# Kernel tuning notes

Hardware: AMD Instinct MI355X
Metric: run time of the kernel (lower is better)

Reference implementation:

```python
import math
import jax, jax.numpy as jnp
import numpy as np

B, C, H, W = 2, 512, 64, 64
HEADS = 8            # channels // num_head_channels = 512 // 64
GROUPS = 32
EPS = 1e-6


def setup_inputs() -> dict:
    key = jax.random.key(0)
    ks = jax.random.split(key, 7)
    x = jax.random.normal(ks[0], (B, C, H, W), dtype=jnp.float32)
    gamma = 1.0 + 0.02 * jax.random.normal(ks[1], (C,), dtype=jnp.float32)
    beta = 0.02 * jax.random.normal(ks[2], (C,), dtype=jnp.float32)
    w_qkv = jax.random.normal(ks[3], (3 * C, C), dtype=jnp.float32) / math.sqrt(C)
    b_qkv = 0.02 * jax.random.normal(ks[4], (3 * C,), dtype=jnp.float32)
    # proj_out is zero-initialized in the module; use small random weights so the
    # op is numerically non-trivial (trained-checkpoint regime)
    w_proj = jax.random.normal(ks[5], (C, C), dtype=jnp.float32) / math.sqrt(C)
    b_proj = 0.02 * jax.random.normal(ks[6], (C,), dtype=jnp.float32)
    return {"x": x, "gamma": gamma, "beta": beta, "w_qkv": w_qkv,
            "b_qkv": b_qkv, "w_proj": w_proj, "b_proj": b_proj}


def reference(x, gamma, beta, w_qkv, b_qkv, w_proj, b_proj):
    b, c, h, w = x.shape
    L = h * w
    xr = x.reshape(b, c, L)

    # GroupNorm(32) over (channels_per_group, spatial)
    xg = xr.reshape(b, GROUPS, c // GROUPS, L)
    mu = jnp.mean(xg, axis=(2, 3), keepdims=True)
    var = jnp.var(xg, axis=(2, 3), keepdims=True)
    xn = ((xg - mu) * jax.lax.rsqrt(var + EPS)).reshape(b, c, L)
    xn = xn * gamma[:, None] + beta[:, None]

    # 1x1 conv QKV: [b, 3c, L]
    qkv = jnp.einsum('oc,bcl->bol', w_qkv, xn) + b_qkv[:, None]

    # QKVAttentionLegacy: reshape [b,3c,L] -> [b*heads, 3*ch, L], split q,k,v
    ch = c // HEADS
    qkv = qkv.reshape(b * HEADS, 3 * ch, L)
    q, k, v = jnp.split(qkv, 3, axis=1)
    scale = 1.0 / math.sqrt(math.sqrt(ch))
    weight = jnp.einsum('bct,bcs->bts', q * scale, k * scale)  # [b*H, L, L]
    weight = jax.nn.softmax(weight.astype(jnp.float32), axis=-1).astype(qkv.dtype)
    a = jnp.einsum('bts,bcs->bct', weight, v).reshape(b, c, L)

    # zero-initialized (here random) 1x1 proj + residual
    hproj = jnp.einsum('oc,bcl->bol', w_proj, a) + b_proj[:, None]
    return (xr + hproj).reshape(b, c, h, w)
```

## Files before the change

### kernel.cpp

```cpp
#include <hip/hip_runtime.h>
#include <stdint.h>


#define LTOK 4096
#define CDIM 512
#define NHEADS 8
#define EPS_GN 1e-6f
#define QKSCALE 0.3535533905932738f
#define QSCL (0.3535533905932738f * 1.44269504088896f)
#define FRAG_BH 262144

typedef float  f4   __attribute__((ext_vector_type(4)));
typedef float  f16v __attribute__((ext_vector_type(16)));
typedef short  bf8  __attribute__((ext_vector_type(8)));
typedef unsigned short u16;
typedef unsigned short u16x8 __attribute__((ext_vector_type(8)));
typedef unsigned short u16x4 __attribute__((ext_vector_type(4)));
typedef uint32_t u32;
typedef uint32_t u32x2 __attribute__((ext_vector_type(2)));
typedef uint32_t u32x4 __attribute__((ext_vector_type(4)));

#define SWZ(row, inrow) ((inrow) ^ (((row)&7)<<4))

__device__ __forceinline__ u16 f2bf(float f){
  uint32_t u = __builtin_bit_cast(uint32_t, f);
  u += 0x7FFFu + ((u>>16)&1u);
  return (u16)(u>>16);
}
__device__ __forceinline__ void gload16(const void* g, void* l){
  __builtin_amdgcn_global_load_lds(
      (const __attribute__((address_space(1))) uint32_t*)g,
      (__attribute__((address_space(3))) uint32_t*)l, 16, 0, 0);
}
__device__ __forceinline__ f4 mfma16(bf8 a, bf8 b, f4 c){
  return __builtin_amdgcn_mfma_f32_16x16x32_bf16(a, b, c, 0, 0, 0);
}
__device__ __forceinline__ f16v mfma32(bf8 a, bf8 b, f16v c){
  return __builtin_amdgcn_mfma_f32_32x32x16_bf16(a, b, c, 0, 0, 0);
}
__device__ __forceinline__ u32 cvtpk(float a, float b){
  u32 d;
  asm("v_cvt_pk_bf16_f32 %0, %1, %2" : "=v"(d) : "v"(a), "v"(b));
  return d;
}

__global__ __launch_bounds__(256) void gn_stats(const float* __restrict__ x,
                                                float* __restrict__ stats){
  const int bg = blockIdx.x;
  const float* p = x + (size_t)bg * 16 * LTOK;
  float s1 = 0.f, s2 = 0.f;
  for (int i = threadIdx.x; i < 16*LTOK/4; i += 256){
    f4 v = ((const f4*)p)[i];
    s1 += v[0]+v[1]+v[2]+v[3];
    s2 += v[0]*v[0]+v[1]*v[1]+v[2]*v[2]+v[3]*v[3];
  }
  #pragma unroll
  for (int off=32; off; off>>=1){ s1 += __shfl_down(s1, off); s2 += __shfl_down(s2, off); }
  __shared__ float a1[4], a2[4];
  const int w = threadIdx.x>>6;
  if ((threadIdx.x&63)==0){ a1[w]=s1; a2[w]=s2; }
  __syncthreads();
  if (threadIdx.x==0){
    float t1 = a1[0]+a1[1]+a1[2]+a1[3];
    float t2 = a2[0]+a2[1]+a2[2]+a2[3];
    const float inv = 1.f/(16.f*LTOK);
    float mu  = t1*inv;
    float var = t2*inv - mu*mu;
    stats[bg*2]   = mu;
    stats[bg*2+1] = rsqrtf(var + EPS_GN);
  }
}

__global__ __launch_bounds__(256) void gn_norm_t(
    const float* __restrict__ x, const float* __restrict__ gamma,
    const float* __restrict__ beta, const float* __restrict__ stats,
    u16* __restrict__ xnT){
  __shared__ float t[64][65];
  const int lb = blockIdx.x*64, cb = blockIdx.y*64, b = blockIdx.z;
  const int tid = threadIdx.x;
  {
    const int cl = tid>>4;
    const int ll = (tid&15)*4;
    #pragma unroll
    for (int rep=0; rep<4; rep++){
      const int cloc = rep*16 + cl;
      const int c = cb + cloc;
      const int grp = c>>4;
      const float mu = stats[(b*32+grp)*2];
      const float rs = stats[(b*32+grp)*2+1];
      const float ga = gamma[c], be = beta[c];
      f4 v = *(const f4*)(x + ((size_t)b*CDIM + c)*LTOK + lb + ll);
      t[cloc][ll+0] = (v[0]-mu)*rs*ga + be;
      t[cloc][ll+1] = (v[1]-mu)*rs*ga + be;
      t[cloc][ll+2] = (v[2]-mu)*rs*ga + be;
      t[cloc][ll+3] = (v[3]-mu)*rs*ga + be;
    }
  }
  __syncthreads();
  {
    const int l2 = tid>>2;
    const int c2 = (tid&3)*16;
    u16x8 o0, o1;
    #pragma unroll
    for (int j=0;j<8;j++){
      o0[j] = f2bf(t[c2+j][l2]);
      o1[j] = f2bf(t[c2+8+j][l2]);
    }
    u16* dst = xnT + ((size_t)b*LTOK + lb + l2)*CDIM + cb + c2;
    *(u16x8*)dst       = o0;
    *((u16x8*)dst + 1) = o1;
  }
}

__global__ __launch_bounds__(256) void cvt_bf16(const float* __restrict__ in,
                                                u16* __restrict__ out, int n4){
  int i = blockIdx.x*256 + threadIdx.x;
  if (i >= n4) return;
  f4 v = ((const f4*)in)[i];
  u16x4 o;
  o[0]=f2bf(v[0]); o[1]=f2bf(v[1]); o[2]=f2bf(v[2]); o[3]=f2bf(v[3]);
  ((u16x4*)out)[i] = o;
}

__global__ __launch_bounds__(256) void qkv_gemm(
    const u16* __restrict__ xnT, const u16* __restrict__ wqkv,
    const float* __restrict__ bqkv,
    u16* __restrict__ qF, u16* __restrict__ kF, u16* __restrict__ vF){
  __shared__ __align__(16) char lA[16384];
  __shared__ __align__(16) char lB[16384];
  const int l0 = blockIdx.x*128, o0 = blockIdx.y*128, b = blockIdx.z;
  const int tid = threadIdx.x, w = tid>>6, lane = tid&63;
  const int wm = w>>1, wn = w&1, fr = lane&15, g = lane>>4;
  f4 acc[4][4] = {};
  const char* Ab = (const char*)(xnT + ((size_t)b*LTOK + l0)*CDIM);
  const char* Bb = (const char*)(wqkv + (size_t)o0*CDIM);
  for (int kt=0; kt<8; kt++){
    #pragma unroll
    for (int j=0;j<4;j++){
      const int off = w*4096 + j*1024 + lane*16;
      const int row = off>>7, inrow = off&127;
      gload16(Ab + (size_t)row*1024 + kt*128 + SWZ(row,inrow), lA + w*4096 + j*1024);
      gload16(Bb + (size_t)row*1024 + kt*128 + SWZ(row,inrow), lB + w*4096 + j*1024);
    }
    __syncthreads();
    bf8 af[4][2], bfr[4][2];
    #pragma unroll
    for (int mt=0;mt<4;mt++){
      #pragma unroll
      for (int kk=0;kk<2;kk++){
        const int row = wm*64 + mt*16 + fr;
        af[mt][kk] = *(const bf8*)(lA + row*128 + SWZ(row, kk*64 + g*16));
      }
    }
    #pragma unroll
    for (int nt=0;nt<4;nt++){
      #pragma unroll
      for (int kk=0;kk<2;kk++){
        const int row = wn*64 + nt*16 + fr;
        bfr[nt][kk] = *(const bf8*)(lB + row*128 + SWZ(row, kk*64 + g*16));
      }
    }
    #pragma unroll
    for (int mt=0;mt<4;mt++){
      #pragma unroll
      for (int nt=0;nt<4;nt++){
        acc[mt][nt] = mfma16(af[mt][0], bfr[nt][0], acc[mt][nt]);
        acc[mt][nt] = mfma16(af[mt][1], bfr[nt][1], acc[mt][nt]);
      }
    }
    __syncthreads();
  }
  #pragma unroll
  for (int nt=0;nt<4;nt++){
    const int o = o0 + wn*64 + nt*16 + fr;
    const float bias = bqkv[o];
    const int head = o / 192;
    int rr = o - head*192;
    const int bh = b*NHEADS + head;
    if (rr < 128){
      u16* base; float sc;
      if (rr < 64){ base = qF; sc = QSCL; }
      else        { base = kF; sc = QKSCALE; rr -= 64; }
      const int sl = rr>>4, hq = (rr>>3)&1, j = rr&7;
      const int Tb = (l0 + wm*64)>>5;
      u16* p = base + (size_t)bh*FRAG_BH + (size_t)(sl*2 + hq)*256 + j;
      #pragma unroll
      for (int mt=0;mt<4;mt++){
        const size_t toff = (size_t)(Tb + (mt>>1))*2048 + (size_t)((mt&1)*16 + g*4)*8;
        #pragma unroll
        for (int r_=0;r_<4;r_++)
          p[toff + r_*8] = f2bf((acc[mt][nt][r_] + bias) * sc);
      }
    } else {
      rr -= 128;
      const int s64 = (l0>>6) + wm;
      u16* p = vF + (size_t)bh*FRAG_BH + (size_t)s64*4096 + (size_t)(g>>1)*512
                  + (size_t)rr*8 + (g&1)*4;
      #pragma unroll
      for (int mt=0;mt<4;mt++){
        u16x4 pk;
        #pragma unroll
        for (int r_=0;r_<4;r_++) pk[r_] = f2bf(acc[mt][nt][r_] + bias);
        *(u16x4*)(p + mt*1024) = pk;
      }
    }
  }
}

__device__ __forceinline__ void loadKF(const u16* kl, int t64, bf8 k0[4], bf8 k1[4]){
  const u16* p = kl + (size_t)t64*4096;
  #pragma unroll
  for (int sl=0; sl<4; sl++){
    k0[sl] = *(const bf8*)(p + sl*512);
    k1[sl] = *(const bf8*)(p + 2048 + sl*512);
  }
}
__device__ __forceinline__ void loadVF(const u16* vl, int t64, bf8 v0[4], bf8 v1[4]){
  const u16* p = vl + (size_t)t64*4096;
  #pragma unroll
  for (int ks=0; ks<4; ks++){
    v0[ks] = *(const bf8*)(p + ks*1024);
    v1[ks] = *(const bf8*)(p + ks*1024 + 256);
  }
}
__device__ __forceinline__ bf8 pfrag(u32 a0, u32 a1, u32 a2, u32 a3, bool hb){
  u32 x0 = (u32)__shfl_xor((int)a2, 32);
  u32 x1 = (u32)__shfl_xor((int)a3, 32);
  u32 x2 = (u32)__shfl_xor((int)a0, 32);
  u32 x3 = (u32)__shfl_xor((int)a1, 32);
  u32x4 w;
  w[0] = hb ? x0 : a0;
  w[1] = hb ? x1 : a1;
  w[2] = hb ? a2 : x2;
  w[3] = hb ? a3 : x3;
  return __builtin_bit_cast(bf8, w);
}

__device__ __forceinline__ void attn_tile(
    const bf8 k0[4], const bf8 k1[4], const bf8 v0[4], const bf8 v1[4],
    const bf8 q[4], f16v& acc0, f16v& acc1, float& m, float& lsum, bool hb){
  f16v SA = {}, SB = {};
  #pragma unroll
  for (int sl=0; sl<4; sl++){
    SA = mfma32(k0[sl], q[sl], SA);
    SB = mfma32(k1[sl], q[sl], SB);
  }
  float t8[8];
  #pragma unroll
  for (int i=0;i<8;i++)
    t8[i] = fmaxf(fmaxf(SA[2*i],SA[2*i+1]), fmaxf(SB[2*i],SB[2*i+1]));
  float mx = fmaxf(fmaxf(fmaxf(t8[0],t8[1]), fmaxf(t8[2],t8[3])),
                   fmaxf(fmaxf(t8[4],t8[5]), fmaxf(t8[6],t8[7])));
  mx = fmaxf(mx, __shfl_xor(mx, 32));
  if (!__all(mx <= m + 8.f)){
    const float mn = fmaxf(m, mx);
    const float crr = exp2f(m - mn);
    m = mn; lsum *= crr;
    #pragma unroll
    for (int i=0;i<16;i++){ acc0[i] *= crr; acc1[i] *= crr; }
  }
  #pragma unroll
  for (int i=0;i<16;i++){ SA[i] = exp2f(SA[i]-m); SB[i] = exp2f(SB[i]-m); }
  float s8[8];
  #pragma unroll
  for (int i=0;i<8;i++)
    s8[i] = (SA[2*i]+SA[2*i+1]) + (SB[2*i]+SB[2*i+1]);
  float ts = ((s8[0]+s8[1])+(s8[2]+s8[3])) + ((s8[4]+s8[5])+(s8[6]+s8[7]));
  ts += __shfl_xor(ts, 32);
  lsum += ts;
  u32 PA[8], PB[8];
  #pragma unroll
  for (int p=0;p<8;p++){
    PA[p] = cvtpk(SA[2*p], SA[2*p+1]);
    PB[p] = cvtpk(SB[2*p], SB[2*p+1]);
  }
  const bf8 pf0 = pfrag(PA[0],PA[1],PA[2],PA[3], hb);
  const bf8 pf1 = pfrag(PA[4],PA[5],PA[6],PA[7], hb);
  const bf8 pf2 = pfrag(PB[0],PB[1],PB[2],PB[3], hb);
  const bf8 pf3 = pfrag(PB[4],PB[5],PB[6],PB[7], hb);
  acc0 = mfma32(v0[0], pf0, acc0);  acc1 = mfma32(v1[0], pf0, acc1);
  acc0 = mfma32(v0[1], pf1, acc0);  acc1 = mfma32(v1[1], pf1, acc1);
  acc0 = mfma32(v0[2], pf2, acc0);  acc1 = mfma32(v1[2], pf2, acc1);
  acc0 = mfma32(v0[3], pf3, acc0);  acc1 = mfma32(v1[3], pf3, acc1);
}

__global__ __launch_bounds__(256,2) void attn4(
    const u16* __restrict__ qF, const u16* __restrict__ kF,
    const u16* __restrict__ vF, u16* __restrict__ aT){
  const int bid = blockIdx.x;
  const int bh = (bid&7)*2 + ((bid>>3)&1);
  const int qt = (bid>>4)*128 + ((threadIdx.x>>6)<<5);
  const int lane = threadIdx.x & 63, r = lane & 31, h = lane>>5;
  const bool hb = h != 0;

  bf8 q[4];
  const u16* qb = qF + (size_t)bh*FRAG_BH + (size_t)(qt>>5)*2048 + h*256 + r*8;
  #pragma unroll
  for (int sl=0; sl<4; sl++) q[sl] = *(const bf8*)(qb + sl*512);

  const u16* kl = kF + (size_t)bh*FRAG_BH + h*256 + r*8;
  const u16* vl = vF + (size_t)bh*FRAG_BH + h*512 + r*8;

  f16v acc0 = {}, acc1 = {};
  float m = -3e38f, lsum = 0.f;

  bf8 kA0[4],kA1[4], kB0[4],kB1[4], v0[4],v1[4];
  loadKF(kl, 0, kA0, kA1);
  for (int t=0; t<64; t+=2){
    loadVF(vl, t, v0, v1);
    loadKF(kl, t+1, kB0, kB1);
    attn_tile(kA0,kA1, v0,v1, q, acc0,acc1, m,lsum, hb);
    loadVF(vl, t+1, v0, v1);
    const int nx = (t+2 < 64) ? t+2 : 0;
    loadKF(kl, nx, kA0, kA1);
    attn_tile(kB0,kB1, v0,v1, q, acc0,acc1, m,lsum, hb);
  }

  const float inv = 1.f/lsum;
  u16* op = aT + ((size_t)bh*LTOK + qt + r)*64;
  #pragma unroll
  for (int qd=0; qd<4; qd++){
    u32x2 w0, w1;
    w0[0] = cvtpk(acc0[4*qd]*inv,   acc0[4*qd+1]*inv);
    w0[1] = cvtpk(acc0[4*qd+2]*inv, acc0[4*qd+3]*inv);
    *(u32x2*)(op + 8*qd + (h?4:0)) = w0;
    w1[0] = cvtpk(acc1[4*qd]*inv,   acc1[4*qd+1]*inv);
    w1[1] = cvtpk(acc1[4*qd+2]*inv, acc1[4*qd+3]*inv);
    *(u32x2*)(op + 32 + 8*qd + (h?4:0)) = w1;
  }
}

__global__ __launch_bounds__(256) void proj_gemm(
    const u16* __restrict__ aT, const u16* __restrict__ wp,
    const float* __restrict__ bp, const float* __restrict__ x,
    float* __restrict__ out){
  __shared__ __align__(16) char lA[16384];
  __shared__ __align__(16) char lB[16384];
  const int l0 = blockIdx.x*128, o0 = blockIdx.y*128, b = blockIdx.z;
  const int tid = threadIdx.x, w = tid>>6, lane = tid&63;
  const int wm = w>>1, wn = w&1, fr = lane&15, g = lane>>4;
  f4 acc[4][4] = {};
  for (int kt=0; kt<8; kt++){
    const char* Ab = (const char*)(wp + (size_t)o0*CDIM + kt*64);
    const char* Bb = (const char*)(aT + ((size_t)(b*NHEADS + kt)*LTOK + l0)*64);
    #pragma unroll
    for (int j=0;j<4;j++){
      const int off = w*4096 + j*1024 + lane*16;
      const int row = off>>7, inrow = off&127;
      gload16(Ab + (size_t)row*1024 + SWZ(row,inrow), lA + w*4096 + j*1024);
      gload16(Bb + (size_t)row*128  + SWZ(row,inrow), lB + w*4096 + j*1024);
    }
    __syncthreads();
    bf8 af[4][2], bfr[4][2];
    #pragma unroll
    for (int mt=0;mt<4;mt++){
      #pragma unroll
      for (int kk=0;kk<2;kk++){
        const int row = wm*64 + mt*16 + fr;
        af[mt][kk] = *(const bf8*)(lA + row*128 + SWZ(row, kk*64 + g*16));
      }
    }
    #pragma unroll
    for (int nt=0;nt<4;nt++){
      #pragma unroll
      for (int kk=0;kk<2;kk++){
        const int row = wn*64 + nt*16 + fr;
        bfr[nt][kk] = *(const bf8*)(lB + row*128 + SWZ(row, kk*64 + g*16));
      }
    }
    #pragma unroll
    for (int mt=0;mt<4;mt++){
      #pragma unroll
      for (int nt=0;nt<4;nt++){
        acc[mt][nt] = mfma16(af[mt][0], bfr[nt][0], acc[mt][nt]);
        acc[mt][nt] = mfma16(af[mt][1], bfr[nt][1], acc[mt][nt]);
      }
    }
    __syncthreads();
  }
  #pragma unroll
  for (int mt=0;mt<4;mt++){
    #pragma unroll
    for (int r=0;r<4;r++){
      const int o = o0 + wm*64 + mt*16 + g*4 + r;
      const float bias = bp[o];
      #pragma unroll
      for (int nt=0;nt<4;nt++){
        const int l = l0 + wn*64 + nt*16 + fr;
        const size_t idx = ((size_t)b*CDIM + o)*LTOK + l;
        out[idx] = x[idx] + bias + acc[mt][nt][r];
      }
    }
  }
}

extern "C" void kernel_launch(void* const* d_in, const int* in_sizes, int n_in,
                              void* d_out, int out_size, void* d_ws, size_t ws_size,
                              hipStream_t stream){
  const float* x     = (const float*)d_in[0];
  const float* gamma = (const float*)d_in[1];
  const float* beta  = (const float*)d_in[2];
  const float* wqkv  = (const float*)d_in[3];
  const float* bqkv  = (const float*)d_in[4];
  const float* wproj = (const float*)d_in[5];
  const float* bproj = (const float*)d_in[6];
  float* out = (float*)d_out;

  char* ws = (char*)d_ws;
  u16* xnT = (u16*)ws;  ws += (size_t)2*LTOK*CDIM*2;
  u16* qF  = (u16*)ws;  ws += (size_t)16*FRAG_BH*2;
  u16* kF  = (u16*)ws;  ws += (size_t)16*FRAG_BH*2;
  u16* vF  = (u16*)ws;  ws += (size_t)16*FRAG_BH*2;
  u16* wqb = (u16*)ws;  ws += (size_t)1536*CDIM*2;
  u16* wpb = (u16*)ws;  ws += (size_t)CDIM*CDIM*2;
  float* stats = (float*)ws; ws += 64*2*sizeof(float);
  u16* aT = xnT;
  if ((size_t)(ws - (char*)d_ws) > ws_size) return;

  gn_stats <<<dim3(64),     dim3(256), 0, stream>>>(x, stats);
  gn_norm_t<<<dim3(64,8,2), dim3(256), 0, stream>>>(x, gamma, beta, stats, xnT);
  cvt_bf16 <<<dim3(768),    dim3(256), 0, stream>>>(wqkv,  wqb, 1536*CDIM/4);
  cvt_bf16 <<<dim3(256),    dim3(256), 0, stream>>>(wproj, wpb, CDIM*CDIM/4);
  qkv_gemm <<<dim3(32,12,2),dim3(256), 0, stream>>>(xnT, wqb, bqkv, qF, kF, vF);
  attn4    <<<dim3(512),    dim3(256), 0, stream>>>(qF, kF, vF, aT);
  proj_gemm<<<dim3(32,4,2), dim3(256), 0, stream>>>(aT, wpb, bproj, x, out);
}
```

Measured before the change: 266.4 us.

## Split attention KV range across warp pairs and merge via shared memory

Each attention block now covers 64 query rows instead of 128. Two wave pairs each process half of the key/value sequence, and the partial softmax states (max, sum, accumulators) are merged through shared memory before normalization and store. This doubles the grid to 1024 blocks and raises the launch-bounds occupancy hint to 4. The goal is better parallelism and latency hiding, at the cost of more total Q-fragment loads, an LDS merge with a barrier, and possible register pressure under the tighter launch bound.

```diff
diff --git a/kernel.cpp b/kernel.cpp
--- a/kernel.cpp
+++ b/kernel.cpp
@@ -284,12 +284,16 @@
   acc0 = mfma32(v0[3], pf3, acc0);  acc1 = mfma32(v1[3], pf3, acc1);
 }
 
-__global__ __launch_bounds__(256,2) void attn4(
+__global__ __launch_bounds__(256,4) void attn5(
     const u16* __restrict__ qF, const u16* __restrict__ kF,
     const u16* __restrict__ vF, u16* __restrict__ aT){
+  __shared__ float lMrg[2*64*35];
   const int bid = blockIdx.x;
   const int bh = (bid&7)*2 + ((bid>>3)&1);
-  const int qt = (bid>>4)*128 + ((threadIdx.x>>6)<<5);
+  const int qc = bid>>4;
+  const int w  = threadIdx.x>>6;
+  const int qt = qc*64 + (w&1)*32;
+  const int shalf = w>>1;
   const int lane = threadIdx.x & 63, r = lane & 31, h = lane>>5;
   const bool hb = h != 0;
 
@@ -304,29 +308,49 @@
   f16v acc0 = {}, acc1 = {};
   float m = -3e38f, lsum = 0.f;
 
+  const int t0 = shalf*32;
   bf8 kA0[4],kA1[4], kB0[4],kB1[4], v0[4],v1[4];
-  loadKF(kl, 0, kA0, kA1);
-  for (int t=0; t<64; t+=2){
+  loadKF(kl, t0, kA0, kA1);
+  for (int t=t0; t<t0+32; t+=2){
     loadVF(vl, t, v0, v1);
     loadKF(kl, t+1, kB0, kB1);
     attn_tile(kA0,kA1, v0,v1, q, acc0,acc1, m,lsum, hb);
     loadVF(vl, t+1, v0, v1);
-    const int nx = (t+2 < 64) ? t+2 : 0;
+    const int nx = (t+2 < t0+32) ? t+2 : t0;
     loadKF(kl, nx, kA0, kA1);
     attn_tile(kB0,kB1, v0,v1, q, acc0,acc1, m,lsum, hb);
   }
 
-  const float inv = 1.f/lsum;
-  u16* op = aT + ((size_t)bh*LTOK + qt + r)*64;
-  #pragma unroll
-  for (int qd=0; qd<4; qd++){
-    u32x2 w0, w1;
-    w0[0] = cvtpk(acc0[4*qd]*inv,   acc0[4*qd+1]*inv);
-    w0[1] = cvtpk(acc0[4*qd+2]*inv, acc0[4*qd+3]*inv);
-    *(u32x2*)(op + 8*qd + (h?4:0)) = w0;
-    w1[0] = cvtpk(acc1[4*qd]*inv,   acc1[4*qd+1]*inv);
-    w1[1] = cvtpk(acc1[4*qd+2]*inv, acc1[4*qd+3]*inv);
-    *(u32x2*)(op + 32 + 8*qd + (h?4:0)) = w1;
+  if (w >= 2){
+    float* dst = lMrg + ((w-2)*64 + lane)*35;
+    dst[0] = m; dst[1] = lsum;
+    #pragma unroll
+    for (int i=0;i<16;i++){ dst[2+i] = acc0[i]; dst[18+i] = acc1[i]; }
+  }
+  __syncthreads();
+  if (w < 2){
+    const float* src = lMrg + (w*64 + lane)*35;
+    const float m2 = src[0], l2 = src[1];
+    const float mN = fmaxf(m, m2);
+    const float cA = exp2f(m - mN), cB = exp2f(m2 - mN);
+    lsum = lsum*cA + l2*cB;
+    #pragma unroll
+    for (int i=0;i<16;i++){
+      acc0[i] = acc0[i]*cA + src[2+i]*cB;
+      acc1[i] = acc1[i]*cA + src[18+i]*cB;
+    }
+    const float inv = 1.f/lsum;
+    u16* op = aT + ((size_t)bh*LTOK + qt + r)*64;
+    #pragma unroll
+    for (int qd=0; qd<4; qd++){
+      u32x2 w0, w1;
+      w0[0] = cvtpk(acc0[4*qd]*inv,   acc0[4*qd+1]*inv);
+      w0[1] = cvtpk(acc0[4*qd+2]*inv, acc0[4*qd+3]*inv);
+      *(u32x2*)(op + 8*qd + (h?4:0)) = w0;
+      w1[0] = cvtpk(acc1[4*qd]*inv,   acc1[4*qd+1]*inv);
+      w1[1] = cvtpk(acc1[4*qd+2]*inv, acc1[4*qd+3]*inv);
+      *(u32x2*)(op + 32 + 8*qd + (h?4:0)) = w1;
+    }
   }
 }
 
@@ -422,6 +446,6 @@
   cvt_bf16 <<<dim3(768),    dim3(256), 0, stream>>>(wqkv,  wqb, 1536*CDIM/4);
   cvt_bf16 <<<dim3(256),    dim3(256), 0, stream>>>(wproj, wpb, CDIM*CDIM/4);
   qkv_gemm <<<dim3(32,12,2),dim3(256), 0, stream>>>(xnT, wqb, bqkv, qF, kF, vF);
-  attn4    <<<dim3(512),    dim3(256), 0, stream>>>(qF, kF, vF, aT);
+  attn5    <<<dim3(1024),   dim3(256), 0, stream>>>(qF, kF, vF, aT);
   proj_gemm<<<dim3(32,4,2), dim3(256), 0, stream>>>(aT, wpb, bproj, x, out);
 }
```

Result: slower. 620.9 us (+133.1%).
